# Kernel tuning notes

Hardware: AMD Instinct MI355X
Metric: run time of the kernel (lower is better)

The kernel has to match this reference:

```python
import jax, jax.numpy as jnp
import numpy as np

V, E, H, L = 256, 256, 1024, 256
B, S = 1024, 256
MAX_LEN = 256
START = 0  # index of '^' start token


def gru_cell(x, h, Wih, Whh, bih, bhh):
    # PyTorch GRU cell: gates ordered (r, z, n)
    gi = x @ Wih.T + bih            # [B, 3H]
    gh = h @ Whh.T + bhh            # [B, 3H]
    ir, iz, inn = jnp.split(gi, 3, axis=-1)
    hr, hz, hn = jnp.split(gh, 3, axis=-1)
    r = jax.nn.sigmoid(ir + hr)
    z = jax.nn.sigmoid(iz + hz)
    n = jnp.tanh(inn + r * hn)
    return (1.0 - z) * n + z * h


def setup_inputs() -> dict:
    key = jax.random.key(0)
    ks = jax.random.split(key, 19)
    p = lambda k, shape: (jax.random.normal(k, shape, jnp.float32) * 0.05)
    return dict(
        x=jax.random.randint(ks[0], (B, S), 0, V),
        eps=jax.random.normal(ks[1], (B, L), jnp.float32),
        embedding=p(ks[2], (V, E)),
        enc_Wih=p(ks[3], (3 * H, E)), enc_Whh=p(ks[4], (3 * H, H)),
        enc_bih=p(ks[5], (3 * H,)), enc_bhh=p(ks[6], (3 * H,)),
        fc_mu_W=p(ks[7], (L, H)), fc_mu_b=p(ks[8], (L,)),
        fc_lv_W=p(ks[9], (L, H)), fc_lv_b=p(ks[10], (L,)),
        l2h_W=p(ks[11], (H, L)), l2h_b=p(ks[12], (H,)),
        dec_Wih=p(ks[13], (3 * H, E)), dec_Whh=p(ks[14], (3 * H, H)),
        dec_bih=p(ks[15], (3 * H,)), dec_bhh=p(ks[16], (3 * H,)),
        out_W=p(ks[17], (V, H)), out_b=p(ks[18], (V,)),
    )


def reference(x, eps, embedding, enc_Wih, enc_Whh, enc_bih, enc_bhh,
              fc_mu_W, fc_mu_b, fc_lv_W, fc_lv_b, l2h_W, l2h_b,
              dec_Wih, dec_Whh, dec_bih, dec_bhh, out_W, out_b):
    Bsz = x.shape[0]
    # ---- encode ----
    emb = embedding[x]                                   # [B, S, E]
    h0 = jnp.zeros((Bsz, enc_Whh.shape[1]), emb.dtype)

    def enc_step(h, xt):
        return gru_cell(xt, h, enc_Wih, enc_Whh, enc_bih, enc_bhh), None

    hT, _ = jax.lax.scan(enc_step, h0, jnp.swapaxes(emb, 0, 1))  # final hidden [B, H]
    mu = hT @ fc_mu_W.T + fc_mu_b
    logvar = hT @ fc_lv_W.T + fc_lv_b
    z = mu + eps * jnp.exp(0.5 * logvar)                 # reparameterize
    h = jnp.tanh(z @ l2h_W.T + l2h_b)                    # [B, H]
    e0 = jnp.broadcast_to(embedding[START], (Bsz, embedding.shape[1]))

    def dec_step(carry, _):
        h, e = carry
        h = gru_cell(e, h, dec_Wih, dec_Whh, dec_bih, dec_bhh)
        logits = h @ out_W.T + out_b                     # [B, V]
        tok = jnp.argmax(logits, axis=1)
        return (h, embedding[tok]), logits

    _, logits = jax.lax.scan(dec_step, (h, e0), None, length=MAX_LEN)
    x_recon = jnp.swapaxes(logits, 0, 1)                 # [B, MAX_LEN, V]
    return x_recon, mu, logvar
```

## Files before the change

kernel.cpp:

```cpp
#include <hip/hip_runtime.h>
#include <stdint.h>
#include <math.h>

typedef _Float16 f16;
typedef __attribute__((ext_vector_type(8))) _Float16 f16x8;
typedef __attribute__((ext_vector_type(4))) float f32x4;
typedef unsigned long long u64;

__device__ __forceinline__ float sigm(float x){ return 1.0f/(1.0f + expf(-x)); }

__global__ __launch_bounds__(256) void split_w(const float* __restrict__ src,
                                               f16* __restrict__ hi, f16* __restrict__ lo, int n){
  int i = blockIdx.x*256 + threadIdx.x;
  if (i >= n) return;
  float x = src[i];
  f16 h = (f16)x;
  float r = x - (float)h;
  hi[i] = h;
  lo[i] = (f16)(r * 2048.0f);
}

__global__ __launch_bounds__(256) void build_tables(
    const float* __restrict__ emb,
    const float* __restrict__ encWih, const float* __restrict__ encBih,
    const float* __restrict__ decWih, const float* __restrict__ decBih,
    float* __restrict__ tabE, float* __restrict__ tabD)
{
  __shared__ float se[256];
  int v = blockIdx.y;
  int col = blockIdx.x*256 + threadIdx.x;
  const float* W  = blockIdx.z ? decWih : encWih;
  const float* bi = blockIdx.z ? decBih : encBih;
  float* tab      = blockIdx.z ? tabD   : tabE;
  se[threadIdx.x] = emb[v*256 + threadIdx.x];
  __syncthreads();
  const float* wr = W + (size_t)col*256;
  float s = 0.f;
  #pragma unroll 8
  for (int k = 0; k < 256; ++k) s += se[k]*wr[k];
  tab[(size_t)v*3072 + col] = s + bi[col];
}

template<int DEC>
__global__ __launch_bounds__(256, 1) void gru_kernel(
    const f16* __restrict__ hHi, const f16* __restrict__ hLo, const float* __restrict__ hOldF,
    const f16* __restrict__ WHi, const f16* __restrict__ WLo,
    const float* __restrict__ bhh, const float* __restrict__ table,
    const int* __restrict__ x, const u64* __restrict__ tokPrev, int t,
    float* __restrict__ hNewF, f16* __restrict__ hNewHi, f16* __restrict__ hNewLo)
{
  __shared__ f16x8 sA[2][2][512];
  __shared__ f16x8 sB[2][2][1536];

  const int raw = blockIdx.x;
  const int j = raw >> 3;
  const int colBlk = (raw & 7)*2 + (j >> 4);
  const int rowBlk = j & 15;

  const int tid  = threadIdx.x;
  const int lane = tid & 63;
  const int wave = tid >> 6;
  const int quad = lane >> 4, lid = lane & 15;
  const int rbase = (wave>>1)*32;
  const int cbase = (wave&1)*32;

  f32x4 accH[3][2][2] = {};
  f32x4 accX[3][2][2] = {};

  int gaOf[2], gbOf[6];
  int laOf[2], lbOf[6];
  #pragma unroll
  for (int i = 0; i < 2; ++i){
    int s = tid + 256*i, row = s >> 3, kk = s & 7;
    gaOf[i] = (rowBlk*64 + row)*1024 + kk*8;
    laOf[i] = row*8 + (kk ^ (row & 7));
  }
  #pragma unroll
  for (int i = 0; i < 6; ++i){
    int s = tid + 256*i, brow = s >> 3, kk = s & 7;
    gbOf[i] = ((brow>>6)*1024 + colBlk*64 + (brow & 63))*1024 + kk*8;
    lbOf[i] = brow*8 + (kk ^ (brow & 7));
  }

  f16x8 stg[16];
#define GLOAD(CK) do{ int k0 = (CK)*64; \
    _Pragma("unroll") for (int i = 0; i < 2; ++i){ \
      stg[i]    = *(const f16x8*)(hHi + gaOf[i] + k0); \
      stg[2+i]  = *(const f16x8*)(hLo + gaOf[i] + k0); } \
    _Pragma("unroll") for (int i = 0; i < 6; ++i){ \
      stg[4+i]  = *(const f16x8*)(WHi + gbOf[i] + k0); \
      stg[10+i] = *(const f16x8*)(WLo + gbOf[i] + k0); } }while(0)

#define SWRITE(BUF) do{ \
    _Pragma("unroll") for (int i = 0; i < 2; ++i){ \
      sA[BUF][0][laOf[i]] = stg[i];   sA[BUF][1][laOf[i]] = stg[2+i]; } \
    _Pragma("unroll") for (int i = 0; i < 6; ++i){ \
      sB[BUF][0][lbOf[i]] = stg[4+i]; sB[BUF][1][lbOf[i]] = stg[10+i]; } }while(0)

  GLOAD(0);
  SWRITE(0);
  __syncthreads();
  GLOAD(1);

  for (int ck = 0; ck < 16; ++ck){
    const int buf = ck & 1;
    #pragma unroll
    for (int ksub = 0; ksub < 2; ++ksub){
      const int kq = ksub*4 + quad;
      f16x8 aH[2], aL[2];
      #pragma unroll
      for (int rt = 0; rt < 2; ++rt){
        int rl = rbase + rt*16 + lid;
        int off = rl*8 + (kq ^ (rl & 7));
        aH[rt] = sA[buf][0][off];
        aL[rt] = sA[buf][1][off];
      }
      f16x8 bH[3][2], bL[3][2];
      #pragma unroll
      for (int g = 0; g < 3; ++g)
        #pragma unroll
        for (int ct = 0; ct < 2; ++ct){
          int bl = g*64 + cbase + ct*16 + lid;
          int off = bl*8 + (kq ^ (bl & 7));
          bH[g][ct] = sB[buf][0][off];
          bL[g][ct] = sB[buf][1][off];
        }
      #pragma unroll
      for (int g = 0; g < 3; ++g)
        #pragma unroll
        for (int rt = 0; rt < 2; ++rt)
          #pragma unroll
          for (int ct = 0; ct < 2; ++ct){
            accH[g][rt][ct] = __builtin_amdgcn_mfma_f32_16x16x32_f16(aH[rt], bH[g][ct], accH[g][rt][ct], 0,0,0);
            accX[g][rt][ct] = __builtin_amdgcn_mfma_f32_16x16x32_f16(aH[rt], bL[g][ct], accX[g][rt][ct], 0,0,0);
            accX[g][rt][ct] = __builtin_amdgcn_mfma_f32_16x16x32_f16(aL[rt], bH[g][ct], accX[g][rt][ct], 0,0,0);
          }
    }
    if (ck < 15){
      SWRITE(buf^1);
      if (ck < 14) GLOAD(ck+2);
    }
    __syncthreads();
  }
#undef GLOAD
#undef SWRITE

  const float s = 1.0f/2048.0f;
  #pragma unroll
  for (int rt = 0; rt < 2; ++rt){
    #pragma unroll
    for (int r = 0; r < 4; ++r){
      int row = rowBlk*64 + rbase + rt*16 + quad*4 + r;
      int tk;
      if (DEC) tk = (t == 0) ? 0 : (255 - (int)(tokPrev[row] & 255));
      else     tk = x[(size_t)row*256 + t] & 255;
      const float* trow = table + (size_t)tk*3072;
      #pragma unroll
      for (int ct = 0; ct < 2; ++ct){
        int col = colBlk*64 + cbase + ct*16 + lid;
        float Cr = accH[0][rt][ct][r] + accX[0][rt][ct][r]*s + bhh[col];
        float Cz = accH[1][rt][ct][r] + accX[1][rt][ct][r]*s + bhh[1024+col];
        float Cn = accH[2][rt][ct][r] + accX[2][rt][ct][r]*s + bhh[2048+col];
        float rg = sigm(trow[col] + Cr);
        float zg = sigm(trow[1024+col] + Cz);
        float ng = tanhf(trow[2048+col] + rg*Cn);
        size_t o = (size_t)row*1024 + col;
        float hv = (1.0f - zg)*ng + zg*hOldF[o];
        hNewF[o] = hv;
        f16 hi = (f16)hv;
        float rr2 = hv - (float)hi;
        hNewHi[o] = hi;
        hNewLo[o] = (f16)(rr2 * 2048.0f);
      }
    }
  }
}

__device__ __forceinline__ u64 akey(float v, int gcol){
  unsigned int b = __float_as_uint(v);
  unsigned int u = (b & 0x80000000u) ? ~b : (b | 0x80000000u);
  return ((u64)u << 8) | (unsigned)(255 - gcol);
}

__global__ __launch_bounds__(256) void logits_argmax(
    const f16* __restrict__ hHi, const f16* __restrict__ hLo,
    const f16* __restrict__ oWHi, const f16* __restrict__ oWLo,
    const float* __restrict__ outB,
    float* __restrict__ outRecon, int t,
    u64* __restrict__ tokCur, u64* __restrict__ tokNext)
{
  __shared__ float lds[16][64];
  const int lane = threadIdx.x & 63;
  const int wave = threadIdx.x >> 6;
  const int quad = lane >> 4, lid = lane & 15;
  const int rowBase = (blockIdx.x >> 2) * 16;
  const int cgrp = blockIdx.x & 3;
  if (cgrp == 0 && threadIdx.x < 16) tokNext[rowBase + threadIdx.x] = 0ull;
  const int colBase = cgrp*64 + wave*16;

  f32x4 accH = {}, accX = {};
  for (int k0 = 0; k0 < 1024; k0 += 32){
    size_t aoff = (size_t)(rowBase + lid)*1024 + k0 + quad*8;
    f16x8 aH = *(const f16x8*)(hHi + aoff);
    f16x8 aL = *(const f16x8*)(hLo + aoff);
    size_t boff = (size_t)(colBase + lid)*1024 + k0 + quad*8;
    f16x8 bH = *(const f16x8*)(oWHi + boff);
    f16x8 bL = *(const f16x8*)(oWLo + boff);
    accH = __builtin_amdgcn_mfma_f32_16x16x32_f16(aH, bH, accH, 0,0,0);
    accX = __builtin_amdgcn_mfma_f32_16x16x32_f16(aH, bL, accX, 0,0,0);
    accX = __builtin_amdgcn_mfma_f32_16x16x32_f16(aL, bH, accX, 0,0,0);
  }
  const float sc = 1.0f/2048.0f;
  const int col = colBase + lid;
  #pragma unroll
  for (int r = 0; r < 4; ++r){
    int rl = quad*4 + r;
    float v = accH[r] + accX[r]*sc + outB[col];
    lds[rl][col - cgrp*64] = v;
    outRecon[(size_t)(rowBase + rl)*65536 + (size_t)t*256 + col] = v;
  }
  __syncthreads();
  #pragma unroll
  for (int rr = 0; rr < 4; ++rr){
    int rl = wave*4 + rr;
    u64 k = akey(lds[rl][lane], cgrp*64 + lane);
    for (int off = 32; off >= 1; off >>= 1){
      u64 o = __shfl_down(k, off, 64);
      if (o > k) k = o;
    }
    if (lane == 0) atomicMax(tokCur + rowBase + rl, k);
  }
}

__global__ __launch_bounds__(256) void latent_a(
    const float* __restrict__ hT,
    const float* __restrict__ muW, const float* __restrict__ muB,
    const float* __restrict__ lvW, const float* __restrict__ lvB,
    const float* __restrict__ eps,
    float* __restrict__ outMu, float* __restrict__ outLv,
    float* __restrict__ z)
{
  __shared__ float sh[1024];
  int b = blockIdx.x, l = threadIdx.x;
  for (int i = l; i < 1024; i += 256) sh[i] = hT[(size_t)b*1024 + i];
  __syncthreads();
  const float* mw = muW + (size_t)l*1024;
  const float* lw = lvW + (size_t)l*1024;
  float sm = 0.f, sv = 0.f;
  #pragma unroll 8
  for (int k = 0; k < 1024; ++k){ float h = sh[k]; sm += h*mw[k]; sv += h*lw[k]; }
  sm += muB[l]; sv += lvB[l];
  float zz = sm + eps[(size_t)b*256 + l] * expf(0.5f*sv);
  outMu[(size_t)b*256 + l] = sm;
  outLv[(size_t)b*256 + l] = sv;
  z[(size_t)b*256 + l] = zz;
}

__global__ __launch_bounds__(256) void latent_b(
    const float* __restrict__ z,
    const float* __restrict__ l2hW, const float* __restrict__ l2hB,
    float* __restrict__ hF, f16* __restrict__ hHi, f16* __restrict__ hLo)
{
  __shared__ float sz[256];
  int b = blockIdx.x;
  int jj = blockIdx.y*256 + threadIdx.x;
  sz[threadIdx.x] = z[(size_t)b*256 + threadIdx.x];
  __syncthreads();
  const float* wr = l2hW + (size_t)jj*256;
  float s = 0.f;
  #pragma unroll 8
  for (int k = 0; k < 256; ++k) s += sz[k]*wr[k];
  float h = tanhf(s + l2hB[jj]);
  size_t o = (size_t)b*1024 + jj;
  hF[o] = h;
  f16 hi = (f16)h;
  float r = h - (float)hi;
  hHi[o] = hi;
  hLo[o] = (f16)(r * 2048.0f);
}

extern "C" void kernel_launch(void* const* d_in, const int* in_sizes, int n_in,
                              void* d_out, int out_size, void* d_ws, size_t ws_size,
                              hipStream_t stream) {
  const int*   x      = (const int*)d_in[0];
  const float* eps    = (const float*)d_in[1];
  const float* emb    = (const float*)d_in[2];
  const float* encWih = (const float*)d_in[3];
  const float* encWhh = (const float*)d_in[4];
  const float* encBih = (const float*)d_in[5];
  const float* encBhh = (const float*)d_in[6];
  const float* muW    = (const float*)d_in[7];
  const float* muB    = (const float*)d_in[8];
  const float* lvW    = (const float*)d_in[9];
  const float* lvB    = (const float*)d_in[10];
  const float* l2hW   = (const float*)d_in[11];
  const float* l2hB   = (const float*)d_in[12];
  const float* decWih = (const float*)d_in[13];
  const float* decWhh = (const float*)d_in[14];
  const float* decBih = (const float*)d_in[15];
  const float* decBhh = (const float*)d_in[16];
  const float* outW   = (const float*)d_in[17];
  const float* outB   = (const float*)d_in[18];

  float* outRecon = (float*)d_out;
  float* outMu    = outRecon + 67108864;
  float* outLv    = outMu + 262144;

  char* ob = (char*)d_out;
  float* tabE   = (float*)(ob + 0);
  f16*   eWHi   = (f16*)(ob + 3145728);
  f16*   eWLo   = (f16*)(ob + 9437184);
  float* zbuf   = (float*)(ob + 15728640);

  char* ws = (char*)d_ws;
  float* tabD   = (float*)(ws + 0);
  f16*   dWHi   = (f16*)(ws + 3145728);
  f16*   dWLo   = (f16*)(ws + 9437184);
  f16*   oWHi   = (f16*)(ws + 15728640);
  f16*   oWLo   = (f16*)(ws + 16252928);
  float* hF[2]  = { (float*)(ws + 16777216), (float*)(ws + 25165824) };
  f16*   hHi[2] = { (f16*)(ws + 20971520),   (f16*)(ws + 29360128) };
  f16*   hLo[2] = { (f16*)(ws + 23068672),   (f16*)(ws + 31457280) };
  u64*   tokb[2]= { (u64*)(ws + 33554432),   (u64*)(ws + 33562624) };

  split_w<<<12288, 256, 0, stream>>>(encWhh, eWHi, eWLo, 3145728);
  split_w<<<12288, 256, 0, stream>>>(decWhh, dWHi, dWLo, 3145728);
  split_w<<<1024, 256, 0, stream>>>(outW, oWHi, oWLo, 262144);

  build_tables<<<dim3(12,256,2), 256, 0, stream>>>(emb, encWih, encBih, decWih, decBih, tabE, tabD);

  hipMemsetAsync(ws + 16777216, 0, 8388608, stream);
  hipMemsetAsync(ws + 33554432, 0, 16384, stream);

  for (int t = 0; t < 256; ++t){
    int a = t & 1, b = a ^ 1;
    gru_kernel<0><<<256, 256, 0, stream>>>(
        hHi[a], hLo[a], hF[a], eWHi, eWLo, encBhh, tabE, x, nullptr, t,
        hF[b], hHi[b], hLo[b]);
  }

  latent_a<<<1024, 256, 0, stream>>>(hF[0], muW, muB, lvW, lvB, eps, outMu, outLv, zbuf);
  latent_b<<<dim3(1024,4), 256, 0, stream>>>(zbuf, l2hW, l2hB, hF[0], hHi[0], hLo[0]);

  for (int t = 0; t < 256; ++t){
    int a = t & 1, b = a ^ 1;
    gru_kernel<1><<<256, 256, 0, stream>>>(
        hHi[a], hLo[a], hF[a], dWHi, dWLo, decBhh, tabD, nullptr, tokb[(t+1)&1], t,
        hF[b], hHi[b], hLo[b]);
    logits_argmax<<<256, 256, 0, stream>>>(
        hHi[b], hLo[b], oWHi, oWLo, outB, outRecon, t, tokb[t&1], tokb[(t+1)&1]);
  }
  (void)in_sizes; (void)n_in; (void)out_size; (void)ws_size;
}
```

Baseline: 24.12 ms.

## Load GRU A operand directly to registers and use nontemporal memory ops

The GRU kernel stops staging the hidden-state (A) tiles through shared memory. Each wave now loads its own A fragments straight from global memory into registers, double-buffered across chunks, and only the weight (B) tiles stay in LDS. Nontemporal loads and stores are also applied to the hidden-state reads and writes and to the logits output, so streaming data is kept from polluting the cache. The trade-off is more redundant global reads of A (the waves sharing the same rows each fetch them) and higher register pressure.

```diff
diff --git a/kernel.cpp b/kernel.cpp
--- a/kernel.cpp
+++ b/kernel.cpp
@@ -8,6 +8,10 @@
 typedef unsigned long long u64;
 
 __device__ __forceinline__ float sigm(float x){ return 1.0f/(1.0f + expf(-x)); }
+
+__device__ __forceinline__ f16x8 ntld(const f16* p){
+  return __builtin_nontemporal_load((const f16x8*)p);
+}
 
 __global__ __launch_bounds__(256) void split_w(const float* __restrict__ src,
                                                f16* __restrict__ hi, f16* __restrict__ lo, int n){
@@ -49,7 +53,6 @@
     const int* __restrict__ x, const u64* __restrict__ tokPrev, int t,
     float* __restrict__ hNewF, f16* __restrict__ hNewHi, f16* __restrict__ hNewLo)
 {
-  __shared__ f16x8 sA[2][2][512];
   __shared__ f16x8 sB[2][2][1536];
 
   const int raw = blockIdx.x;
@@ -67,14 +70,7 @@
   f32x4 accH[3][2][2] = {};
   f32x4 accX[3][2][2] = {};
 
-  int gaOf[2], gbOf[6];
-  int laOf[2], lbOf[6];
-  #pragma unroll
-  for (int i = 0; i < 2; ++i){
-    int s = tid + 256*i, row = s >> 3, kk = s & 7;
-    gaOf[i] = (rowBlk*64 + row)*1024 + kk*8;
-    laOf[i] = row*8 + (kk ^ (row & 7));
-  }
+  int gbOf[6], lbOf[6];
   #pragma unroll
   for (int i = 0; i < 6; ++i){
     int s = tid + 256*i, brow = s >> 3, kk = s & 7;
@@ -82,68 +78,69 @@
     lbOf[i] = brow*8 + (kk ^ (brow & 7));
   }
 
-  f16x8 stg[16];
-#define GLOAD(CK) do{ int k0 = (CK)*64; \
-    _Pragma("unroll") for (int i = 0; i < 2; ++i){ \
-      stg[i]    = *(const f16x8*)(hHi + gaOf[i] + k0); \
-      stg[2+i]  = *(const f16x8*)(hLo + gaOf[i] + k0); } \
+  int aOf[2];
+  #pragma unroll
+  for (int rt = 0; rt < 2; ++rt)
+    aOf[rt] = (rowBlk*64 + rbase + rt*16 + lid)*1024 + quad*8;
+
+  f16x8 stg[12];
+#define BGLOAD(CK) do{ int k0 = (CK)*64; \
     _Pragma("unroll") for (int i = 0; i < 6; ++i){ \
-      stg[4+i]  = *(const f16x8*)(WHi + gbOf[i] + k0); \
-      stg[10+i] = *(const f16x8*)(WLo + gbOf[i] + k0); } }while(0)
-
-#define SWRITE(BUF) do{ \
-    _Pragma("unroll") for (int i = 0; i < 2; ++i){ \
-      sA[BUF][0][laOf[i]] = stg[i];   sA[BUF][1][laOf[i]] = stg[2+i]; } \
+      stg[i]   = *(const f16x8*)(WHi + gbOf[i] + k0); \
+      stg[6+i] = *(const f16x8*)(WLo + gbOf[i] + k0); } }while(0)
+
+#define BSWRITE(BUF) do{ \
     _Pragma("unroll") for (int i = 0; i < 6; ++i){ \
-      sB[BUF][0][lbOf[i]] = stg[4+i]; sB[BUF][1][lbOf[i]] = stg[10+i]; } }while(0)
-
-  GLOAD(0);
-  SWRITE(0);
-  __syncthreads();
-  GLOAD(1);
-
-  for (int ck = 0; ck < 16; ++ck){
-    const int buf = ck & 1;
-    #pragma unroll
-    for (int ksub = 0; ksub < 2; ++ksub){
-      const int kq = ksub*4 + quad;
-      f16x8 aH[2], aL[2];
-      #pragma unroll
-      for (int rt = 0; rt < 2; ++rt){
-        int rl = rbase + rt*16 + lid;
-        int off = rl*8 + (kq ^ (rl & 7));
-        aH[rt] = sA[buf][0][off];
-        aL[rt] = sA[buf][1][off];
-      }
-      f16x8 bH[3][2], bL[3][2];
-      #pragma unroll
-      for (int g = 0; g < 3; ++g)
-        #pragma unroll
-        for (int ct = 0; ct < 2; ++ct){
-          int bl = g*64 + cbase + ct*16 + lid;
-          int off = bl*8 + (kq ^ (bl & 7));
-          bH[g][ct] = sB[buf][0][off];
-          bL[g][ct] = sB[buf][1][off];
-        }
-      #pragma unroll
-      for (int g = 0; g < 3; ++g)
-        #pragma unroll
-        for (int rt = 0; rt < 2; ++rt)
-          #pragma unroll
-          for (int ct = 0; ct < 2; ++ct){
-            accH[g][rt][ct] = __builtin_amdgcn_mfma_f32_16x16x32_f16(aH[rt], bH[g][ct], accH[g][rt][ct], 0,0,0);
-            accX[g][rt][ct] = __builtin_amdgcn_mfma_f32_16x16x32_f16(aH[rt], bL[g][ct], accX[g][rt][ct], 0,0,0);
-            accX[g][rt][ct] = __builtin_amdgcn_mfma_f32_16x16x32_f16(aL[rt], bH[g][ct], accX[g][rt][ct], 0,0,0);
-          }
-    }
-    if (ck < 15){
-      SWRITE(buf^1);
-      if (ck < 14) GLOAD(ck+2);
-    }
+      sB[BUF][0][lbOf[i]] = stg[i]; sB[BUF][1][lbOf[i]] = stg[6+i]; } }while(0)
+
+#define ALOAD(DST, CK) do{ int k0 = (CK)*64; \
+    _Pragma("unroll") for (int ks = 0; ks < 2; ++ks) \
+      _Pragma("unroll") for (int rt = 0; rt < 2; ++rt){ \
+        DST[ks][0][rt] = ntld(hHi + aOf[rt] + k0 + ks*32); \
+        DST[ks][1][rt] = ntld(hLo + aOf[rt] + k0 + ks*32); } }while(0)
+
+#define COMPUTE(BUF, AC) do{ \
+    _Pragma("unroll") for (int ksub = 0; ksub < 2; ++ksub){ \
+      const int kq = ksub*4 + quad; \
+      f16x8 bH[3][2], bL[3][2]; \
+      _Pragma("unroll") for (int g = 0; g < 3; ++g) \
+        _Pragma("unroll") for (int ct = 0; ct < 2; ++ct){ \
+          int bl = g*64 + cbase + ct*16 + lid; \
+          int off = bl*8 + (kq ^ (bl & 7)); \
+          bH[g][ct] = sB[BUF][0][off]; \
+          bL[g][ct] = sB[BUF][1][off]; } \
+      _Pragma("unroll") for (int g = 0; g < 3; ++g) \
+        _Pragma("unroll") for (int rt = 0; rt < 2; ++rt) \
+          _Pragma("unroll") for (int ct = 0; ct < 2; ++ct){ \
+            accH[g][rt][ct] = __builtin_amdgcn_mfma_f32_16x16x32_f16(AC[ksub][0][rt], bH[g][ct], accH[g][rt][ct], 0,0,0); \
+            accX[g][rt][ct] = __builtin_amdgcn_mfma_f32_16x16x32_f16(AC[ksub][0][rt], bL[g][ct], accX[g][rt][ct], 0,0,0); \
+            accX[g][rt][ct] = __builtin_amdgcn_mfma_f32_16x16x32_f16(AC[ksub][1][rt], bH[g][ct], accX[g][rt][ct], 0,0,0); } \
+    } }while(0)
+
+  f16x8 aP[2][2][2], aQ[2][2][2];
+
+  BGLOAD(0);
+  BSWRITE(0);
+  ALOAD(aP, 0);
+  __syncthreads();
+  BGLOAD(1);
+
+  for (int ck2 = 0; ck2 < 16; ck2 += 2){
+    ALOAD(aQ, ck2+1);
+    COMPUTE(0, aP);
+    BSWRITE(1);
+    if (ck2 < 14) BGLOAD(ck2+2);
     __syncthreads();
-  }
-#undef GLOAD
-#undef SWRITE
+    if (ck2 < 14) ALOAD(aP, ck2+2);
+    COMPUTE(1, aQ);
+    if (ck2 < 14) BSWRITE(0);
+    if (ck2 < 13) BGLOAD(ck2+3);
+    __syncthreads();
+  }
+#undef BGLOAD
+#undef BSWRITE
+#undef ALOAD
+#undef COMPUTE
 
   const float s = 1.0f/2048.0f;
   #pragma unroll
@@ -165,12 +162,12 @@
         float zg = sigm(trow[1024+col] + Cz);
         float ng = tanhf(trow[2048+col] + rg*Cn);
         size_t o = (size_t)row*1024 + col;
-        float hv = (1.0f - zg)*ng + zg*hOldF[o];
-        hNewF[o] = hv;
+        float hv = (1.0f - zg)*ng + zg*__builtin_nontemporal_load(hOldF + o);
+        __builtin_nontemporal_store(hv, hNewF + o);
         f16 hi = (f16)hv;
         float rr2 = hv - (float)hi;
-        hNewHi[o] = hi;
-        hNewLo[o] = (f16)(rr2 * 2048.0f);
+        __builtin_nontemporal_store(hi, hNewHi + o);
+        __builtin_nontemporal_store((f16)(rr2 * 2048.0f), hNewLo + o);
       }
     }
   }
@@ -201,8 +198,8 @@
   f32x4 accH = {}, accX = {};
   for (int k0 = 0; k0 < 1024; k0 += 32){
     size_t aoff = (size_t)(rowBase + lid)*1024 + k0 + quad*8;
-    f16x8 aH = *(const f16x8*)(hHi + aoff);
-    f16x8 aL = *(const f16x8*)(hLo + aoff);
+    f16x8 aH = ntld(hHi + aoff);
+    f16x8 aL = ntld(hLo + aoff);
     size_t boff = (size_t)(colBase + lid)*1024 + k0 + quad*8;
     f16x8 bH = *(const f16x8*)(oWHi + boff);
     f16x8 bL = *(const f16x8*)(oWLo + boff);
@@ -217,7 +214,7 @@
     int rl = quad*4 + r;
     float v = accH[r] + accX[r]*sc + outB[col];
     lds[rl][col - cgrp*64] = v;
-    outRecon[(size_t)(rowBase + rl)*65536 + (size_t)t*256 + col] = v;
+    __builtin_nontemporal_store(v, outRecon + (size_t)(rowBase + rl)*65536 + (size_t)t*256 + col);
   }
   __syncthreads();
   #pragma unroll
```

New measurement: 32.60 ms. 1.35x slower.
